# Optimization experiments

Hardware: AMD Instinct MI355X
Metric: run time of the kernel (lower is better)

The kernel has to match this reference:

```python
import jax, jax.numpy as jnp
import numpy as np

HEADS = 8
DIM_HEAD = 64
SCALE = DIM_HEAD ** -0.5


def setup_inputs() -> dict:
    key = jax.random.key(0)
    k1, k2, k3, k4 = jax.random.split(key, 4)
    b, dim, l = 4, 512, 2048
    hidden = HEADS * DIM_HEAD  # 512
    x = jax.random.normal(k1, (b, dim, l), dtype=jnp.float32)
    w_qkv = jax.random.normal(k2, (3 * hidden, dim), dtype=jnp.float32) * (dim ** -0.5)
    w_out = jax.random.normal(k3, (dim, hidden), dtype=jnp.float32) * (hidden ** -0.5)
    b_out = jax.random.normal(k4, (dim,), dtype=jnp.float32) * 0.01
    return {"x": x, "w_qkv": w_qkv, "w_out": w_out, "b_out": b_out}


def reference(x, w_qkv, w_out, b_out):
    b, c, l = x.shape
    h, d = HEADS, DIM_HEAD
    # 1x1 Conv1d == channel matmul: [3*hidden, c] x [b, c, l] -> [b, 3*hidden, l]
    qkv = jnp.einsum('oc,bcl->bol', w_qkv, x)
    q, k, v = jnp.split(qkv, 3, axis=1)
    # 'b (h d) l -> b h d l'
    q = q.reshape(b, h, d, l) * SCALE
    k = k.reshape(b, h, d, l)
    v = v.reshape(b, h, d, l)
    sim = jnp.einsum('bhdi,bhdj->bhij', q, k)          # [b, h, l, l]
    attn = jax.nn.softmax(sim, axis=-1)
    out = jnp.einsum('bhij,bhdj->bhid', attn, v)       # [b, h, l, d]
    # 'b h l d -> b (h d) l'
    out = out.transpose(0, 1, 3, 2).reshape(b, h * d, l)
    return jnp.einsum('oc,bcl->bol', w_out, out) + b_out[None, :, None]
```

## Files before the change

kernel.cpp:

```cpp
#include <hip/hip_runtime.h>

#define L_SEQ 2048
#define KDIM  512

typedef __attribute__((ext_vector_type(8))) short short8v;
typedef __attribute__((ext_vector_type(4))) float f32x4;
typedef __attribute__((ext_vector_type(16))) float f32x16;
typedef __attribute__((ext_vector_type(4))) unsigned u32x4;

static __device__ __forceinline__ short f2b(float f) {
    union { float f; unsigned u; } v; v.f = f;
    unsigned r = v.u + 0x7fffu + ((v.u >> 16) & 1u);
    return (short)(r >> 16);
}

static __device__ __forceinline__ float fast_exp2(float x) {
#if __has_builtin(__builtin_amdgcn_exp2f)
    return __builtin_amdgcn_exp2f(x);
#else
    return exp2f(x);
#endif
}

static __device__ __forceinline__ void gl2lds16(const short* g, short* l) {
    __builtin_amdgcn_global_load_lds(
        (const __attribute__((address_space(1))) unsigned*)g,
        (__attribute__((address_space(3))) unsigned*)l,
        16, 0, 0);
}

__global__ __launch_bounds__(256) void prep(
    const float* __restrict__ wq, const float* __restrict__ wo,
    const float* __restrict__ x,
    short* __restrict__ wqb, short* __restrict__ wob, short* __restrict__ xT)
{
    __shared__ __align__(16) float T[64 * 72];
    const int t = threadIdx.x;
    int bid = blockIdx.x;

    if (bid < 1024) {
        const int i = bid * 256 + t;
        const int NQ = 1536 * 512 / 4;
        float4 v;
        if (i < NQ) v = ((const float4*)wq)[i];
        else        v = ((const float4*)wo)[i - NQ];
        short4 s;
        s.x = f2b(v.x); s.y = f2b(v.y); s.z = f2b(v.z); s.w = f2b(v.w);
        if (i < NQ) ((short4*)wqb)[i] = s;
        else        ((short4*)wob)[i - NQ] = s;
        return;
    }
    bid -= 1024;
    const int l0 = (bid & 31) * 64;
    const int c0 = ((bid >> 5) & 7) * 64;
    const int b  = bid >> 8;

#pragma unroll
    for (int j = 0; j < 4; ++j) {
        const int idx = j * 256 + t;
        const int row = idx >> 4, c4 = idx & 15;
        const float4 v = *(const float4*)&x[((size_t)b * KDIM + c0 + row) * L_SEQ + l0 + c4 * 4];
        *(float4*)&T[row * 72 + c4 * 4] = v;
    }
    __syncthreads();

#pragma unroll
    for (int j = 0; j < 2; ++j) {
        const int idx = j * 256 + t;
        const int l = idx >> 3, ch = idx & 7;
        short8v s;
#pragma unroll
        for (int e = 0; e < 8; ++e)
            s[e] = f2b(T[(ch * 8 + e) * 72 + l]);
        *(short8v*)&xT[((size_t)b * L_SEQ + l0 + l) * KDIM + c0 + ch * 8] = s;
    }
}

template<int EPI>
__global__ __launch_bounds__(256) void gemm_bt(
    const short* __restrict__ Ag, const short* __restrict__ Bbase,
    const float* __restrict__ bias,
    short* __restrict__ Qws, short* __restrict__ Kws, short* __restrict__ Vws,
    float* __restrict__ Cout)
{
    constexpr int TO   = (EPI == 0) ? 128 : 64;
    constexpr int WO   = TO / 2;
    constexpr int NI   = WO / 16;
    constexpr int CA   = TO * 64 * 2 / 1024;
    constexpr int CB   = 16;
    constexpr int CPW  = (CA + CB) / 4;
    constexpr int SMEM = (EPI == 0) ? 34816 : 24576;

    const int bz = blockIdx.z;
    const int o0 = blockIdx.y * TO;
    const int l0 = blockIdx.x * 128;
    const short* Bg = Bbase + (size_t)bz * L_SEQ * KDIM;

    __shared__ __align__(16) char smem[SMEM];
    short* sA = (short*)smem;
    short* sB = (short*)(smem + TO * 64 * 2);

    const int t    = threadIdx.x;
    const int w    = t >> 6;
    const int lane = t & 63;
    const int quad = lane >> 4;
    const int l16  = lane & 15;
    const int wo   = (w & 1) * WO;
    const int wl   = (w >> 1) * 64;

    f32x4 acc[NI][4];
#pragma unroll
    for (int i = 0; i < NI; ++i)
#pragma unroll
        for (int n = 0; n < 4; ++n) acc[i][n] = (f32x4){0,0,0,0};

    const int lrow = lane >> 3;
    const int lcol = (lane & 7) * 8;

    for (int k0 = 0; k0 < KDIM; k0 += 64) {
#pragma unroll
        for (int p = 0; p < CPW; ++p) {
            const int cid = w * CPW + p;
            if (cid < CA) {
                const int row = cid * 8 + lrow;
                gl2lds16(Ag + (size_t)(o0 + row) * KDIM + k0 + lcol, sA + cid * 512);
            } else {
                const int row = (cid - CA) * 8 + lrow;
                gl2lds16(Bg + (size_t)(l0 + row) * KDIM + k0 + lcol, sB + (cid - CA) * 512);
            }
        }
        __syncthreads();

#pragma unroll
        for (int ks = 0; ks < 2; ++ks) {
            short8v af[NI], bf[4];
#pragma unroll
            for (int i = 0; i < NI; ++i)
                af[i] = *(const short8v*)&sA[(wo + i * 16 + l16) * 64 + ks * 32 + quad * 8];
#pragma unroll
            for (int n = 0; n < 4; ++n)
                bf[n] = *(const short8v*)&sB[(wl + n * 16 + l16) * 64 + ks * 32 + quad * 8];
#pragma unroll
            for (int i = 0; i < NI; ++i)
#pragma unroll
                for (int n = 0; n < 4; ++n)
                    acc[i][n] = __builtin_amdgcn_mfma_f32_16x16x32_bf16(af[i], bf[n], acc[i][n], 0, 0, 0);
        }
        __syncthreads();
    }

    if (EPI == 0) {
        const int type  = o0 >> 9;
        const int local = o0 & 511;
        const int bh0   = bz * 8 + (local >> 6);
        const float sc  = (type == 0) ? 0.18033688011112042f : 1.0f;
        short* T = (short*)smem;

        if (type == 2) {
#pragma unroll
            for (int i = 0; i < NI; ++i)
#pragma unroll
                for (int n = 0; n < 4; ++n)
#pragma unroll
                    for (int r = 0; r < 4; ++r)
                        T[(wo + i * 16 + quad * 4 + r) * 136 + wl + n * 16 + l16] =
                            f2b(acc[i][n][r]);
            __syncthreads();
#pragma unroll
            for (int p = 0; p < 8; ++p) {
                const int idx = p * 256 + t;
                const int o = idx >> 4, c = idx & 15;
                const float4 v = *(const float4*)&T[o * 136 + c * 8];
                short* dst = Vws + ((size_t)(bh0 + (o >> 6)) * 64 + (o & 63)) * L_SEQ + l0 + c * 8;
                *(float4*)dst = v;
            }
        } else {
#pragma unroll
            for (int i = 0; i < NI; ++i)
#pragma unroll
                for (int n = 0; n < 4; ++n) {
                    short4 s;
                    s.x = f2b(acc[i][n][0] * sc);
                    s.y = f2b(acc[i][n][1] * sc);
                    s.z = f2b(acc[i][n][2] * sc);
                    s.w = f2b(acc[i][n][3] * sc);
                    *(short4*)&T[(wl + n * 16 + l16) * 136 + wo + i * 16 + quad * 4] = s;
                }
            __syncthreads();
            short* base = (type == 0) ? Qws : Kws;
#pragma unroll
            for (int p = 0; p < 8; ++p) {
                const int idx = p * 256 + t;
                const int l = idx >> 4, c = idx & 15;
                const float4 v = *(const float4*)&T[l * 136 + c * 8];
                short* dst = base + ((size_t)(bh0 + (c >> 3)) * L_SEQ + l0 + l) * 64 + (c & 7) * 8;
                *(float4*)dst = v;
            }
        }
    } else {
        float* Cb = Cout + (size_t)bz * KDIM * L_SEQ;
#pragma unroll
        for (int i = 0; i < NI; ++i) {
            const int o = o0 + wo + i * 16 + quad * 4;
            float bv[4];
#pragma unroll
            for (int r = 0; r < 4; ++r) bv[r] = bias[o + r];
#pragma unroll
            for (int n = 0; n < 4; ++n) {
                const int l = l0 + wl + n * 16 + l16;
#pragma unroll
                for (int r = 0; r < 4; ++r)
                    Cb[(size_t)(o + r) * L_SEQ + l] = acc[i][n][r] + bv[r];
            }
        }
    }
}

__global__ __launch_bounds__(512, 4) void attn_mfma(
    const short* __restrict__ Qws, const short* __restrict__ Kws,
    const short* __restrict__ Vws, short* __restrict__ ao)
{
    const int bh = blockIdx.x & 31;
    const int b  = bh >> 3;
    const int h  = bh & 7;
    const int i0 = (blockIdx.x >> 5) * 128;

    __shared__ __align__(16) char smem[36864];
    float* Old = (float*)smem;

    const int t    = threadIdx.x;
    const int w    = t >> 6;
    const int lane = t & 63;
    const int l31  = lane & 31;
    const int hi   = lane >> 5;
    const int gi   = w >> 1;
    const int jh   = w & 1;

    const short* Qb = Qws + (size_t)bh * L_SEQ * 64;
    const short* Kb = Kws + (size_t)bh * L_SEQ * 64;
    const short* Vb = Vws + (size_t)bh * 64 * L_SEQ;

    short8v qa[4];
#pragma unroll
    for (int dk = 0; dk < 4; ++dk)
        qa[dk] = *(const short8v*)(Qb + (size_t)(i0 + gi * 32 + l31) * 64 + dk * 16 + hi * 8);

    f32x16 oacc0, oacc1;
#pragma unroll
    for (int e = 0; e < 16; ++e) { oacc0[e] = 0.f; oacc1[e] = 0.f; }
    float rsum = 0.f;

    const int r = t >> 3, c = t & 7;

    {
        short* K0 = (short*)smem;
        short* V0 = (short*)(smem + 9216);
        const float4 k0 = *(const float4*)(Kb + (size_t)r * 64 + c * 8);
        const float4 v0 = *(const float4*)(Vb + (size_t)r * L_SEQ + c * 8);
        *(float4*)&K0[r * 72 + c * 8] = k0;
        *(float4*)&V0[r * 72 + c * 8] = v0;
    }
    __syncthreads();

    for (int jt = 0; jt < L_SEQ / 64; ++jt) {
        const int j0 = jt * 64;
        const short* Kc = (const short*)(smem + (jt & 1) * 18432);
        const short* Vc = (const short*)(smem + (jt & 1) * 18432 + 9216);
        const bool more = (jt + 1 < L_SEQ / 64);

        float4 nk, nv;
        if (more) {
            nk = *(const float4*)(Kb + (size_t)(j0 + 64 + r) * 64 + c * 8);
            nv = *(const float4*)(Vb + (size_t)r * L_SEQ + j0 + 64 + c * 8);
        }

        f32x16 sacc;
#pragma unroll
        for (int e = 0; e < 16; ++e) sacc[e] = 0.f;
#pragma unroll
        for (int dk = 0; dk < 4; ++dk) {
            const short8v kf = *(const short8v*)&Kc[(jh * 32 + l31) * 72 + dk * 16 + hi * 8];
            sacc = __builtin_amdgcn_mfma_f32_32x32x16_bf16(kf, qa[dk], sacc, 0, 0, 0);
        }

        float p[16];
#pragma unroll
        for (int e = 0; e < 16; ++e) p[e] = fast_exp2(sacc[e]);
#pragma unroll
        for (int e = 0; e < 16; e += 4)
            rsum += (p[e] + p[e + 1]) + (p[e + 2] + p[e + 3]);

        unsigned wv[8];
#pragma unroll
        for (int g = 0; g < 4; ++g) {
            wv[2 * g]     = __builtin_amdgcn_perm(__float_as_uint(p[4 * g + 1]),
                                                  __float_as_uint(p[4 * g]),     0x07060302u);
            wv[2 * g + 1] = __builtin_amdgcn_perm(__float_as_uint(p[4 * g + 3]),
                                                  __float_as_uint(p[4 * g + 2]), 0x07060302u);
        }
        unsigned xv[8];
#pragma unroll
        for (int k = 0; k < 8; ++k)
            xv[k] = (unsigned)__shfl_xor((int)wv[k], 32, 64);

        u32x4 f0, f1;
        f0[0] = hi ? xv[2] : wv[0];  f0[1] = hi ? xv[3] : wv[1];
        f0[2] = hi ? wv[2] : xv[0];  f0[3] = hi ? wv[3] : xv[1];
        f1[0] = hi ? xv[6] : wv[4];  f1[1] = hi ? xv[7] : wv[5];
        f1[2] = hi ? wv[6] : xv[4];  f1[3] = hi ? wv[7] : xv[5];
        const short8v pa0 = __builtin_bit_cast(short8v, f0);
        const short8v pa1 = __builtin_bit_cast(short8v, f1);

        {
            const short8v vf00 = *(const short8v*)&Vc[(0 * 32 + l31) * 72 + jh * 32 + 0 * 16 + hi * 8];
            const short8v vf01 = *(const short8v*)&Vc[(1 * 32 + l31) * 72 + jh * 32 + 0 * 16 + hi * 8];
            oacc0 = __builtin_amdgcn_mfma_f32_32x32x16_bf16(pa0, vf00, oacc0, 0, 0, 0);
            oacc1 = __builtin_amdgcn_mfma_f32_32x32x16_bf16(pa0, vf01, oacc1, 0, 0, 0);
            const short8v vf10 = *(const short8v*)&Vc[(0 * 32 + l31) * 72 + jh * 32 + 1 * 16 + hi * 8];
            const short8v vf11 = *(const short8v*)&Vc[(1 * 32 + l31) * 72 + jh * 32 + 1 * 16 + hi * 8];
            oacc0 = __builtin_amdgcn_mfma_f32_32x32x16_bf16(pa1, vf10, oacc0, 0, 0, 0);
            oacc1 = __builtin_amdgcn_mfma_f32_32x32x16_bf16(pa1, vf11, oacc1, 0, 0, 0);
        }

        if (more) {
            short* Kn = (short*)(smem + ((jt & 1) ^ 1) * 18432);
            short* Vn = (short*)(smem + ((jt & 1) ^ 1) * 18432 + 9216);
            *(float4*)&Kn[r * 72 + c * 8] = nk;
            *(float4*)&Vn[r * 72 + c * 8] = nv;
        }
        __syncthreads();
    }

    const float r2 = rsum + __shfl_xor(rsum, 32, 64);

    float* Opart = (float*)smem;
    float* Rp    = (float*)(smem + 32768);

    if (jh == 1) {
#pragma unroll
        for (int q = 0; q < 4; ++q) {
            float4 a = { oacc0[4 * q], oacc0[4 * q + 1], oacc0[4 * q + 2], oacc0[4 * q + 3] };
            float4 bq = { oacc1[4 * q], oacc1[4 * q + 1], oacc1[4 * q + 2], oacc1[4 * q + 3] };
            *(float4*)&Opart[gi * 2048 + q * 256 + lane * 4]         = a;
            *(float4*)&Opart[gi * 2048 + (4 + q) * 256 + lane * 4]   = bq;
        }
        if (hi == 0) Rp[gi * 32 + l31] = r2;
    }
    __syncthreads();

    if (jh == 0) {
#pragma unroll
        for (int q = 0; q < 4; ++q) {
            const float4 a  = *(const float4*)&Opart[gi * 2048 + q * 256 + lane * 4];
            const float4 bq = *(const float4*)&Opart[gi * 2048 + (4 + q) * 256 + lane * 4];
            oacc0[4 * q] += a.x;  oacc0[4 * q + 1] += a.y;
            oacc0[4 * q + 2] += a.z; oacc0[4 * q + 3] += a.w;
            oacc1[4 * q] += bq.x; oacc1[4 * q + 1] += bq.y;
            oacc1[4 * q + 2] += bq.z; oacc1[4 * q + 3] += bq.w;
        }
        const float rt  = r2 + Rp[gi * 32 + l31];
        const float inv = 1.0014f / rt;
#pragma unroll
        for (int e = 0; e < 16; ++e) {
            const int rowi = (e & 3) + 8 * (e >> 2) + 4 * hi;
            const float iv = __shfl(inv, rowi, 64);
            oacc0[e] *= iv;
            oacc1[e] *= iv;
        }
    }
    __syncthreads();

    if (jh == 0) {
#pragma unroll
        for (int e = 0; e < 16; ++e) {
            const int rowi = (e & 3) + 8 * (e >> 2) + 4 * hi;
            Old[(gi * 32 + rowi) * 68 + l31]      = oacc0[e];
            Old[(gi * 32 + rowi) * 68 + 32 + l31] = oacc1[e];
        }
    }
    __syncthreads();

#pragma unroll
    for (int p = 0; p < 4; ++p) {
        const int idx = p * 512 + t;
        const int i = idx >> 4, c4 = idx & 15;
        const float4 v = *(const float4*)&Old[i * 68 + c4 * 4];
        short4 s;
        s.x = f2b(v.x); s.y = f2b(v.y); s.z = f2b(v.z); s.w = f2b(v.w);
        *(short4*)&ao[((size_t)b * L_SEQ + i0 + i) * KDIM + h * 64 + c4 * 4] = s;
    }
}

extern "C" void kernel_launch(void* const* d_in, const int* in_sizes, int n_in,
                              void* d_out, int out_size, void* d_ws, size_t ws_size,
                              hipStream_t stream)
{
    const float* x     = (const float*)d_in[0];
    const float* w_qkv = (const float*)d_in[1];
    const float* w_out = (const float*)d_in[2];
    const float* b_out = (const float*)d_in[3];
    float* out = (float*)d_out;

    char* ws = (char*)d_ws;
    short* xT    = (short*)ws;                      ws += (size_t)4 * L_SEQ * KDIM * 2;
    short* wq_bf = (short*)ws;                      ws += (size_t)1536 * 512 * 2;
    short* wo_bf = (short*)ws;                      ws += (size_t)512 * 512 * 2;
    short* Qws   = (short*)ws;                      ws += (size_t)32 * L_SEQ * 64 * 2;
    short* Kws   = (short*)ws;                      ws += (size_t)32 * L_SEQ * 64 * 2;
    short* Vws   = (short*)ws;                      ws += (size_t)32 * L_SEQ * 64 * 2;
    short* ao    = (short*)ws;

    dim3 blk(256);
    prep       <<<dim3(2048), blk, 0, stream>>>(w_qkv, w_out, x, wq_bf, wo_bf, xT);
    gemm_bt<0> <<<dim3(16, 12, 4), blk, 0, stream>>>(wq_bf, xT, nullptr, Qws, Kws, Vws, nullptr);
    attn_mfma  <<<dim3(512), dim3(512), 0, stream>>>(Qws, Kws, Vws, ao);
    gemm_bt<1> <<<dim3(16, 8, 4), blk, 0, stream>>>(wo_bf, ao, b_out, nullptr, nullptr, nullptr, out);
}
```

Measured before the change: 162.1 us.

## Software-pipeline attention loop with triple-buffered K/V and one-step-ahead QK

Restructures the attention inner loop so that each step computes the QK^T scores for the next tile while doing exp and PV for the current one. K/V staging moves from a double buffer to a triple buffer with a two-tile prefetch distance. The loop is unrolled by six so the buffer rotation is fixed at compile time. The goal is to overlap MFMA work with exp/shuffle work and to hide global load latency. In exchange, LDS grows from 36 KB to 54 KB per block and register pressure rises, which may cut occupancy under launch_bounds(512,4).

```diff
diff --git a/kernel.cpp b/kernel.cpp
--- a/kernel.cpp
+++ b/kernel.cpp
@@ -216,6 +216,83 @@
     }
 }
 
+template<bool DO_QK, bool DO_STAGE>
+static __device__ __forceinline__ void attn_step(
+    const int jt,
+    const short* __restrict__ bQK,
+    const short* __restrict__ bPV,
+    short* __restrict__ bW,
+    const short* __restrict__ Kb, const short* __restrict__ Vb,
+    const short8v (&qa)[4],
+    f32x16& sC, f32x16& sN,
+    f32x16& oacc0, f32x16& oacc1, float& rsum,
+    const int r, const int c, const int l31, const int hi, const int jh)
+{
+    float4 nk, nv;
+    if (DO_STAGE) {
+        nk = *(const float4*)(Kb + (size_t)((jt + 2) * 64 + r) * 64 + c * 8);
+        nv = *(const float4*)(Vb + (size_t)r * L_SEQ + (jt + 2) * 64 + c * 8);
+    }
+
+    if (DO_QK) {
+        f32x16 s;
+#pragma unroll
+        for (int e = 0; e < 16; ++e) s[e] = 0.f;
+#pragma unroll
+        for (int dk = 0; dk < 4; ++dk) {
+            const short8v kf = *(const short8v*)&bQK[(jh * 32 + l31) * 72 + dk * 16 + hi * 8];
+            s = __builtin_amdgcn_mfma_f32_32x32x16_bf16(kf, qa[dk], s, 0, 0, 0);
+        }
+        sN = s;
+    }
+
+    float p[16];
+#pragma unroll
+    for (int e = 0; e < 16; ++e) p[e] = fast_exp2(sC[e]);
+#pragma unroll
+    for (int e = 0; e < 16; e += 4)
+        rsum += (p[e] + p[e + 1]) + (p[e + 2] + p[e + 3]);
+
+    unsigned wv[8];
+#pragma unroll
+    for (int g = 0; g < 4; ++g) {
+        wv[2 * g]     = __builtin_amdgcn_perm(__float_as_uint(p[4 * g + 1]),
+                                              __float_as_uint(p[4 * g]),     0x07060302u);
+        wv[2 * g + 1] = __builtin_amdgcn_perm(__float_as_uint(p[4 * g + 3]),
+                                              __float_as_uint(p[4 * g + 2]), 0x07060302u);
+    }
+    unsigned xv[8];
+#pragma unroll
+    for (int k = 0; k < 8; ++k)
+        xv[k] = (unsigned)__shfl_xor((int)wv[k], 32, 64);
+
+    u32x4 f0, f1;
+    f0[0] = hi ? xv[2] : wv[0];  f0[1] = hi ? xv[3] : wv[1];
+    f0[2] = hi ? wv[2] : xv[0];  f0[3] = hi ? wv[3] : xv[1];
+    f1[0] = hi ? xv[6] : wv[4];  f1[1] = hi ? xv[7] : wv[5];
+    f1[2] = hi ? wv[6] : xv[4];  f1[3] = hi ? wv[7] : xv[5];
+    const short8v pa0 = __builtin_bit_cast(short8v, f0);
+    const short8v pa1 = __builtin_bit_cast(short8v, f1);
+
+    const short* Vc = bPV + 4608;
+    {
+        const short8v vf00 = *(const short8v*)&Vc[(0 * 32 + l31) * 72 + jh * 32 + 0 * 16 + hi * 8];
+        const short8v vf01 = *(const short8v*)&Vc[(1 * 32 + l31) * 72 + jh * 32 + 0 * 16 + hi * 8];
+        oacc0 = __builtin_amdgcn_mfma_f32_32x32x16_bf16(pa0, vf00, oacc0, 0, 0, 0);
+        oacc1 = __builtin_amdgcn_mfma_f32_32x32x16_bf16(pa0, vf01, oacc1, 0, 0, 0);
+        const short8v vf10 = *(const short8v*)&Vc[(0 * 32 + l31) * 72 + jh * 32 + 1 * 16 + hi * 8];
+        const short8v vf11 = *(const short8v*)&Vc[(1 * 32 + l31) * 72 + jh * 32 + 1 * 16 + hi * 8];
+        oacc0 = __builtin_amdgcn_mfma_f32_32x32x16_bf16(pa1, vf10, oacc0, 0, 0, 0);
+        oacc1 = __builtin_amdgcn_mfma_f32_32x32x16_bf16(pa1, vf11, oacc1, 0, 0, 0);
+    }
+
+    if (DO_STAGE) {
+        *(float4*)&bW[r * 72 + c * 8]        = nk;
+        *(float4*)&bW[4608 + r * 72 + c * 8] = nv;
+    }
+    __syncthreads();
+}
+
 __global__ __launch_bounds__(512, 4) void attn_mfma(
     const short* __restrict__ Qws, const short* __restrict__ Kws,
     const short* __restrict__ Vws, short* __restrict__ ao)
@@ -225,7 +302,10 @@
     const int h  = bh & 7;
     const int i0 = (blockIdx.x >> 5) * 128;
 
-    __shared__ __align__(16) char smem[36864];
+    __shared__ __align__(16) char smem[55296];
+    short* B0 = (short*)smem;
+    short* B1 = (short*)(smem + 18432);
+    short* B2 = (short*)(smem + 36864);
     float* Old = (float*)smem;
 
     const int t    = threadIdx.x;
@@ -253,83 +333,37 @@
     const int r = t >> 3, c = t & 7;
 
     {
-        short* K0 = (short*)smem;
-        short* V0 = (short*)(smem + 9216);
         const float4 k0 = *(const float4*)(Kb + (size_t)r * 64 + c * 8);
         const float4 v0 = *(const float4*)(Vb + (size_t)r * L_SEQ + c * 8);
-        *(float4*)&K0[r * 72 + c * 8] = k0;
-        *(float4*)&V0[r * 72 + c * 8] = v0;
-    }
-    __syncthreads();
-
-    for (int jt = 0; jt < L_SEQ / 64; ++jt) {
-        const int j0 = jt * 64;
-        const short* Kc = (const short*)(smem + (jt & 1) * 18432);
-        const short* Vc = (const short*)(smem + (jt & 1) * 18432 + 9216);
-        const bool more = (jt + 1 < L_SEQ / 64);
-
-        float4 nk, nv;
-        if (more) {
-            nk = *(const float4*)(Kb + (size_t)(j0 + 64 + r) * 64 + c * 8);
-            nv = *(const float4*)(Vb + (size_t)r * L_SEQ + j0 + 64 + c * 8);
-        }
-
-        f32x16 sacc;
-#pragma unroll
-        for (int e = 0; e < 16; ++e) sacc[e] = 0.f;
-#pragma unroll
-        for (int dk = 0; dk < 4; ++dk) {
-            const short8v kf = *(const short8v*)&Kc[(jh * 32 + l31) * 72 + dk * 16 + hi * 8];
-            sacc = __builtin_amdgcn_mfma_f32_32x32x16_bf16(kf, qa[dk], sacc, 0, 0, 0);
-        }
-
-        float p[16];
-#pragma unroll
-        for (int e = 0; e < 16; ++e) p[e] = fast_exp2(sacc[e]);
-#pragma unroll
-        for (int e = 0; e < 16; e += 4)
-            rsum += (p[e] + p[e + 1]) + (p[e + 2] + p[e + 3]);
-
-        unsigned wv[8];
-#pragma unroll
-        for (int g = 0; g < 4; ++g) {
-            wv[2 * g]     = __builtin_amdgcn_perm(__float_as_uint(p[4 * g + 1]),
-                                                  __float_as_uint(p[4 * g]),     0x07060302u);
-            wv[2 * g + 1] = __builtin_amdgcn_perm(__float_as_uint(p[4 * g + 3]),
-                                                  __float_as_uint(p[4 * g + 2]), 0x07060302u);
-        }
-        unsigned xv[8];
-#pragma unroll
-        for (int k = 0; k < 8; ++k)
-            xv[k] = (unsigned)__shfl_xor((int)wv[k], 32, 64);
-
-        u32x4 f0, f1;
-        f0[0] = hi ? xv[2] : wv[0];  f0[1] = hi ? xv[3] : wv[1];
-        f0[2] = hi ? wv[2] : xv[0];  f0[3] = hi ? wv[3] : xv[1];
-        f1[0] = hi ? xv[6] : wv[4];  f1[1] = hi ? xv[7] : wv[5];
-        f1[2] = hi ? wv[6] : xv[4];  f1[3] = hi ? wv[7] : xv[5];
-        const short8v pa0 = __builtin_bit_cast(short8v, f0);
-        const short8v pa1 = __builtin_bit_cast(short8v, f1);
-
-        {
-            const short8v vf00 = *(const short8v*)&Vc[(0 * 32 + l31) * 72 + jh * 32 + 0 * 16 + hi * 8];
-            const short8v vf01 = *(const short8v*)&Vc[(1 * 32 + l31) * 72 + jh * 32 + 0 * 16 + hi * 8];
-            oacc0 = __builtin_amdgcn_mfma_f32_32x32x16_bf16(pa0, vf00, oacc0, 0, 0, 0);
-            oacc1 = __builtin_amdgcn_mfma_f32_32x32x16_bf16(pa0, vf01, oacc1, 0, 0, 0);
-            const short8v vf10 = *(const short8v*)&Vc[(0 * 32 + l31) * 72 + jh * 32 + 1 * 16 + hi * 8];
-            const short8v vf11 = *(const short8v*)&Vc[(1 * 32 + l31) * 72 + jh * 32 + 1 * 16 + hi * 8];
-            oacc0 = __builtin_amdgcn_mfma_f32_32x32x16_bf16(pa1, vf10, oacc0, 0, 0, 0);
-            oacc1 = __builtin_amdgcn_mfma_f32_32x32x16_bf16(pa1, vf11, oacc1, 0, 0, 0);
-        }
-
-        if (more) {
-            short* Kn = (short*)(smem + ((jt & 1) ^ 1) * 18432);
-            short* Vn = (short*)(smem + ((jt & 1) ^ 1) * 18432 + 9216);
-            *(float4*)&Kn[r * 72 + c * 8] = nk;
-            *(float4*)&Vn[r * 72 + c * 8] = nv;
-        }
-        __syncthreads();
-    }
+        const float4 k1 = *(const float4*)(Kb + (size_t)(64 + r) * 64 + c * 8);
+        const float4 v1 = *(const float4*)(Vb + (size_t)r * L_SEQ + 64 + c * 8);
+        *(float4*)&B0[r * 72 + c * 8]        = k0;
+        *(float4*)&B0[4608 + r * 72 + c * 8] = v0;
+        *(float4*)&B1[r * 72 + c * 8]        = k1;
+        *(float4*)&B1[4608 + r * 72 + c * 8] = v1;
+    }
+    __syncthreads();
+
+    f32x16 sA, sB;
+#pragma unroll
+    for (int e = 0; e < 16; ++e) sA[e] = 0.f;
+#pragma unroll
+    for (int dk = 0; dk < 4; ++dk) {
+        const short8v kf = *(const short8v*)&B0[(jh * 32 + l31) * 72 + dk * 16 + hi * 8];
+        sA = __builtin_amdgcn_mfma_f32_32x32x16_bf16(kf, qa[dk], sA, 0, 0, 0);
+    }
+
+    for (int p6 = 0; p6 < 5; ++p6) {
+        const int t6 = p6 * 6;
+        attn_step<true, true>(t6 + 0, B1, B0, B2, Kb, Vb, qa, sA, sB, oacc0, oacc1, rsum, r, c, l31, hi, jh);
+        attn_step<true, true>(t6 + 1, B2, B1, B0, Kb, Vb, qa, sB, sA, oacc0, oacc1, rsum, r, c, l31, hi, jh);
+        attn_step<true, true>(t6 + 2, B0, B2, B1, Kb, Vb, qa, sA, sB, oacc0, oacc1, rsum, r, c, l31, hi, jh);
+        attn_step<true, true>(t6 + 3, B1, B0, B2, Kb, Vb, qa, sB, sA, oacc0, oacc1, rsum, r, c, l31, hi, jh);
+        attn_step<true, true>(t6 + 4, B2, B1, B0, Kb, Vb, qa, sA, sB, oacc0, oacc1, rsum, r, c, l31, hi, jh);
+        attn_step<true, true>(t6 + 5, B0, B2, B1, Kb, Vb, qa, sB, sA, oacc0, oacc1, rsum, r, c, l31, hi, jh);
+    }
+    attn_step<true,  false>(30, B1, B0, B2, Kb, Vb, qa, sA, sB, oacc0, oacc1, rsum, r, c, l31, hi, jh);
+    attn_step<false, false>(31, B2, B1, B0, Kb, Vb, qa, sB, sA, oacc0, oacc1, rsum, r, c, l31, hi, jh);
 
     const float r2 = rsum + __shfl_xor(rsum, 32, 64);
 
```

New measurement: 162.1 us. About the same (-0.0%).

## Double query rows per attention wave, use permlane32 swap, and XCD-swizzle GEMM grid

Applied to the files above, without the earlier changes.

The attention kernel moves from 512 to 256 threads per block, with each wave handling two 32-row query tiles. This reuses every K and V LDS fragment across two MFMA chains and halves LDS traffic per FLOP. The cross-half-wave exchange of P values now uses v_permlane32_swap instead of shfl_xor plus selects. Both GEMM launches become 1D grids with an XCD-aware block remap so neighbouring tiles share L2. The cost is more accumulator registers per wave (four 32x32 outputs) and lower occupancy bounds.

```diff
diff --git a/kernel.cpp b/kernel.cpp
--- a/kernel.cpp
+++ b/kernel.cpp
@@ -90,10 +90,18 @@
     constexpr int CB   = 16;
     constexpr int CPW  = (CA + CB) / 4;
     constexpr int SMEM = (EPI == 0) ? 34816 : 24576;
-
-    const int bz = blockIdx.z;
-    const int o0 = blockIdx.y * TO;
-    const int l0 = blockIdx.x * 128;
+    constexpr int NY   = (EPI == 0) ? 12 : 8;
+    constexpr int CPX  = 16 * NY * 4 / 8;
+
+    const int o   = blockIdx.x;
+    const int wsw = (o & 7) * CPX + (o >> 3);
+    const int xb  = wsw / (NY * 4);
+    const int rem = wsw % (NY * 4);
+    const int bz  = rem / NY;
+    const int yb  = rem % NY;
+
+    const int o0 = yb * TO;
+    const int l0 = xb * 128;
     const short* Bg = Bbase + (size_t)bz * L_SEQ * KDIM;
 
     __shared__ __align__(16) char smem[SMEM];
@@ -160,7 +168,7 @@
 #pragma unroll
             for (int i = 0; i < NI; ++i)
 #pragma unroll
-                for (int n = 0; n < 4; ++n)
+            for (int n = 0; n < 4; ++n)
 #pragma unroll
                     for (int r = 0; r < 4; ++r)
                         T[(wo + i * 16 + quad * 4 + r) * 136 + wl + n * 16 + l16] =
@@ -169,9 +177,9 @@
 #pragma unroll
             for (int p = 0; p < 8; ++p) {
                 const int idx = p * 256 + t;
-                const int o = idx >> 4, c = idx & 15;
-                const float4 v = *(const float4*)&T[o * 136 + c * 8];
-                short* dst = Vws + ((size_t)(bh0 + (o >> 6)) * 64 + (o & 63)) * L_SEQ + l0 + c * 8;
+                const int oo = idx >> 4, cc = idx & 15;
+                const float4 v = *(const float4*)&T[oo * 136 + cc * 8];
+                short* dst = Vws + ((size_t)(bh0 + (oo >> 6)) * 64 + (oo & 63)) * L_SEQ + l0 + cc * 8;
                 *(float4*)dst = v;
             }
         } else {
@@ -191,9 +199,9 @@
 #pragma unroll
             for (int p = 0; p < 8; ++p) {
                 const int idx = p * 256 + t;
-                const int l = idx >> 4, c = idx & 15;
-                const float4 v = *(const float4*)&T[l * 136 + c * 8];
-                short* dst = base + ((size_t)(bh0 + (c >> 3)) * L_SEQ + l0 + l) * 64 + (c & 7) * 8;
+                const int l = idx >> 4, cc = idx & 15;
+                const float4 v = *(const float4*)&T[l * 136 + cc * 8];
+                short* dst = base + ((size_t)(bh0 + (cc >> 3)) * L_SEQ + l0 + l) * 64 + (cc & 7) * 8;
                 *(float4*)dst = v;
             }
         }
@@ -201,22 +209,26 @@
         float* Cb = Cout + (size_t)bz * KDIM * L_SEQ;
 #pragma unroll
         for (int i = 0; i < NI; ++i) {
-            const int o = o0 + wo + i * 16 + quad * 4;
+            const int oo = o0 + wo + i * 16 + quad * 4;
             float bv[4];
 #pragma unroll
-            for (int r = 0; r < 4; ++r) bv[r] = bias[o + r];
+            for (int r = 0; r < 4; ++r) bv[r] = bias[oo + r];
 #pragma unroll
             for (int n = 0; n < 4; ++n) {
                 const int l = l0 + wl + n * 16 + l16;
 #pragma unroll
                 for (int r = 0; r < 4; ++r)
-                    Cb[(size_t)(o + r) * L_SEQ + l] = acc[i][n][r] + bv[r];
-            }
-        }
-    }
-}
-
-__global__ __launch_bounds__(512, 4) void attn_mfma(
+                    Cb[(size_t)(oo + r) * L_SEQ + l] = acc[i][n][r] + bv[r];
+            }
+        }
+    }
+}
+
+static __device__ __forceinline__ void plswap(unsigned& a, unsigned& b) {
+    asm("v_permlane32_swap_b32 %0, %1" : "+v"(a), "+v"(b));
+}
+
+__global__ __launch_bounds__(256, 2) void attn_mfma(
     const short* __restrict__ Qws, const short* __restrict__ Kws,
     const short* __restrict__ Vws, short* __restrict__ ao)
 {
@@ -240,25 +252,34 @@
     const short* Kb = Kws + (size_t)bh * L_SEQ * 64;
     const short* Vb = Vws + (size_t)bh * 64 * L_SEQ;
 
-    short8v qa[4];
-#pragma unroll
-    for (int dk = 0; dk < 4; ++dk)
-        qa[dk] = *(const short8v*)(Qb + (size_t)(i0 + gi * 32 + l31) * 64 + dk * 16 + hi * 8);
-
-    f32x16 oacc0, oacc1;
-#pragma unroll
-    for (int e = 0; e < 16; ++e) { oacc0[e] = 0.f; oacc1[e] = 0.f; }
-    float rsum = 0.f;
-
-    const int r = t >> 3, c = t & 7;
+    short8v qa[2][4];
+#pragma unroll
+    for (int it = 0; it < 2; ++it)
+#pragma unroll
+        for (int dk = 0; dk < 4; ++dk)
+            qa[it][dk] = *(const short8v*)(Qb +
+                (size_t)(i0 + gi * 64 + it * 32 + l31) * 64 + dk * 16 + hi * 8);
+
+    f32x16 o00, o01, o10, o11;
+#pragma unroll
+    for (int e = 0; e < 16; ++e) { o00[e] = 0.f; o01[e] = 0.f; o10[e] = 0.f; o11[e] = 0.f; }
+    float rsum0 = 0.f, rsum1 = 0.f;
+
+    const int r = t >> 2, c = t & 3;
 
     {
         short* K0 = (short*)smem;
         short* V0 = (short*)(smem + 9216);
-        const float4 k0 = *(const float4*)(Kb + (size_t)r * 64 + c * 8);
-        const float4 v0 = *(const float4*)(Vb + (size_t)r * L_SEQ + c * 8);
-        *(float4*)&K0[r * 72 + c * 8] = k0;
-        *(float4*)&V0[r * 72 + c * 8] = v0;
+        const short* kg = Kb + (size_t)r * 64 + c * 16;
+        const short* vg = Vb + (size_t)r * L_SEQ + c * 16;
+        const float4 k0 = *(const float4*)kg;
+        const float4 k1 = *(const float4*)(kg + 8);
+        const float4 v0 = *(const float4*)vg;
+        const float4 v1 = *(const float4*)(vg + 8);
+        *(float4*)&K0[r * 72 + c * 16]     = k0;
+        *(float4*)&K0[r * 72 + c * 16 + 8] = k1;
+        *(float4*)&V0[r * 72 + c * 16]     = v0;
+        *(float4*)&V0[r * 72 + c * 16 + 8] = v1;
     }
     __syncthreads();
 
@@ -268,70 +289,106 @@
         const short* Vc = (const short*)(smem + (jt & 1) * 18432 + 9216);
         const bool more = (jt + 1 < L_SEQ / 64);
 
-        float4 nk, nv;
+        float4 nk0, nk1, nv0, nv1;
         if (more) {
-            nk = *(const float4*)(Kb + (size_t)(j0 + 64 + r) * 64 + c * 8);
-            nv = *(const float4*)(Vb + (size_t)r * L_SEQ + j0 + 64 + c * 8);
-        }
-
-        f32x16 sacc;
-#pragma unroll
-        for (int e = 0; e < 16; ++e) sacc[e] = 0.f;
+            const short* kg = Kb + (size_t)(j0 + 64 + r) * 64 + c * 16;
+            const short* vg = Vb + (size_t)r * L_SEQ + j0 + 64 + c * 16;
+            nk0 = *(const float4*)kg;
+            nk1 = *(const float4*)(kg + 8);
+            nv0 = *(const float4*)vg;
+            nv1 = *(const float4*)(vg + 8);
+        }
+
+        f32x16 s0, s1;
+#pragma unroll
+        for (int e = 0; e < 16; ++e) { s0[e] = 0.f; s1[e] = 0.f; }
 #pragma unroll
         for (int dk = 0; dk < 4; ++dk) {
             const short8v kf = *(const short8v*)&Kc[(jh * 32 + l31) * 72 + dk * 16 + hi * 8];
-            sacc = __builtin_amdgcn_mfma_f32_32x32x16_bf16(kf, qa[dk], sacc, 0, 0, 0);
-        }
-
-        float p[16];
-#pragma unroll
-        for (int e = 0; e < 16; ++e) p[e] = fast_exp2(sacc[e]);
-#pragma unroll
-        for (int e = 0; e < 16; e += 4)
-            rsum += (p[e] + p[e + 1]) + (p[e + 2] + p[e + 3]);
-
-        unsigned wv[8];
-#pragma unroll
-        for (int g = 0; g < 4; ++g) {
-            wv[2 * g]     = __builtin_amdgcn_perm(__float_as_uint(p[4 * g + 1]),
-                                                  __float_as_uint(p[4 * g]),     0x07060302u);
-            wv[2 * g + 1] = __builtin_amdgcn_perm(__float_as_uint(p[4 * g + 3]),
-                                                  __float_as_uint(p[4 * g + 2]), 0x07060302u);
-        }
-        unsigned xv[8];
-#pragma unroll
-        for (int k = 0; k < 8; ++k)
-            xv[k] = (unsigned)__shfl_xor((int)wv[k], 32, 64);
-
-        u32x4 f0, f1;
-        f0[0] = hi ? xv[2] : wv[0];  f0[1] = hi ? xv[3] : wv[1];
-        f0[2] = hi ? wv[2] : xv[0];  f0[3] = hi ? wv[3] : xv[1];
-        f1[0] = hi ? xv[6] : wv[4];  f1[1] = hi ? xv[7] : wv[5];
-        f1[2] = hi ? wv[6] : xv[4];  f1[3] = hi ? wv[7] : xv[5];
-        const short8v pa0 = __builtin_bit_cast(short8v, f0);
-        const short8v pa1 = __builtin_bit_cast(short8v, f1);
-
+            s0 = __builtin_amdgcn_mfma_f32_32x32x16_bf16(kf, qa[0][dk], s0, 0, 0, 0);
+            s1 = __builtin_amdgcn_mfma_f32_32x32x16_bf16(kf, qa[1][dk], s1, 0, 0, 0);
+        }
+
+        short8v pa00, pa01, pa10, pa11;
         {
-            const short8v vf00 = *(const short8v*)&Vc[(0 * 32 + l31) * 72 + jh * 32 + 0 * 16 + hi * 8];
-            const short8v vf01 = *(const short8v*)&Vc[(1 * 32 + l31) * 72 + jh * 32 + 0 * 16 + hi * 8];
-            oacc0 = __builtin_amdgcn_mfma_f32_32x32x16_bf16(pa0, vf00, oacc0, 0, 0, 0);
-            oacc1 = __builtin_amdgcn_mfma_f32_32x32x16_bf16(pa0, vf01, oacc1, 0, 0, 0);
-            const short8v vf10 = *(const short8v*)&Vc[(0 * 32 + l31) * 72 + jh * 32 + 1 * 16 + hi * 8];
-            const short8v vf11 = *(const short8v*)&Vc[(1 * 32 + l31) * 72 + jh * 32 + 1 * 16 + hi * 8];
-            oacc0 = __builtin_amdgcn_mfma_f32_32x32x16_bf16(pa1, vf10, oacc0, 0, 0, 0);
-            oacc1 = __builtin_amdgcn_mfma_f32_32x32x16_bf16(pa1, vf11, oacc1, 0, 0, 0);
+            float p[16];
+#pragma unroll
+            for (int e = 0; e < 16; ++e) p[e] = fast_exp2(s0[e]);
+#pragma unroll
+            for (int e = 0; e < 16; e += 4)
+                rsum0 += (p[e] + p[e + 1]) + (p[e + 2] + p[e + 3]);
+            unsigned wv[8];
+#pragma unroll
+            for (int g = 0; g < 4; ++g) {
+                wv[2 * g]     = __builtin_amdgcn_perm(__float_as_uint(p[4 * g + 1]),
+                                                      __float_as_uint(p[4 * g]),     0x07060302u);
+                wv[2 * g + 1] = __builtin_amdgcn_perm(__float_as_uint(p[4 * g + 3]),
+                                                      __float_as_uint(p[4 * g + 2]), 0x07060302u);
+            }
+            unsigned a0 = wv[0], a2 = wv[2]; plswap(a0, a2);
+            unsigned a1 = wv[1], a3 = wv[3]; plswap(a1, a3);
+            unsigned b0 = wv[4], b2 = wv[6]; plswap(b0, b2);
+            unsigned b1 = wv[5], b3 = wv[7]; plswap(b1, b3);
+            u32x4 f0, f1;
+            f0[0] = a0; f0[1] = a1; f0[2] = a2; f0[3] = a3;
+            f1[0] = b0; f1[1] = b1; f1[2] = b2; f1[3] = b3;
+            pa00 = __builtin_bit_cast(short8v, f0);
+            pa01 = __builtin_bit_cast(short8v, f1);
+        }
+        {
+            float p[16];
+#pragma unroll
+            for (int e = 0; e < 16; ++e) p[e] = fast_exp2(s1[e]);
+#pragma unroll
+            for (int e = 0; e < 16; e += 4)
+                rsum1 += (p[e] + p[e + 1]) + (p[e + 2] + p[e + 3]);
+            unsigned wv[8];
+#pragma unroll
+            for (int g = 0; g < 4; ++g) {
+                wv[2 * g]     = __builtin_amdgcn_perm(__float_as_uint(p[4 * g + 1]),
+                                                      __float_as_uint(p[4 * g]),     0x07060302u);
+                wv[2 * g + 1] = __builtin_amdgcn_perm(__float_as_uint(p[4 * g + 3]),
+                                                      __float_as_uint(p[4 * g + 2]), 0x07060302u);
+            }
+            unsigned a0 = wv[0], a2 = wv[2]; plswap(a0, a2);
+            unsigned a1 = wv[1], a3 = wv[3]; plswap(a1, a3);
+            unsigned b0 = wv[4], b2 = wv[6]; plswap(b0, b2);
+            unsigned b1 = wv[5], b3 = wv[7]; plswap(b1, b3);
+            u32x4 f0, f1;
+            f0[0] = a0; f0[1] = a1; f0[2] = a2; f0[3] = a3;
+            f1[0] = b0; f1[1] = b1; f1[2] = b2; f1[3] = b3;
+            pa10 = __builtin_bit_cast(short8v, f0);
+            pa11 = __builtin_bit_cast(short8v, f1);
+        }
+
+        {
+            const short8v v00 = *(const short8v*)&Vc[(0 * 32 + l31) * 72 + jh * 32 + 0 * 16 + hi * 8];
+            o00 = __builtin_amdgcn_mfma_f32_32x32x16_bf16(pa00, v00, o00, 0, 0, 0);
+            o10 = __builtin_amdgcn_mfma_f32_32x32x16_bf16(pa10, v00, o10, 0, 0, 0);
+            const short8v v10 = *(const short8v*)&Vc[(1 * 32 + l31) * 72 + jh * 32 + 0 * 16 + hi * 8];
+            o01 = __builtin_amdgcn_mfma_f32_32x32x16_bf16(pa00, v10, o01, 0, 0, 0);
+            o11 = __builtin_amdgcn_mfma_f32_32x32x16_bf16(pa10, v10, o11, 0, 0, 0);
+            const short8v v01 = *(const short8v*)&Vc[(0 * 32 + l31) * 72 + jh * 32 + 1 * 16 + hi * 8];
+            o00 = __builtin_amdgcn_mfma_f32_32x32x16_bf16(pa01, v01, o00, 0, 0, 0);
+            o10 = __builtin_amdgcn_mfma_f32_32x32x16_bf16(pa11, v01, o10, 0, 0, 0);
+            const short8v v11 = *(const short8v*)&Vc[(1 * 32 + l31) * 72 + jh * 32 + 1 * 16 + hi * 8];
+            o01 = __builtin_amdgcn_mfma_f32_32x32x16_bf16(pa01, v11, o01, 0, 0, 0);
+            o11 = __builtin_amdgcn_mfma_f32_32x32x16_bf16(pa11, v11, o11, 0, 0, 0);
         }
 
         if (more) {
             short* Kn = (short*)(smem + ((jt & 1) ^ 1) * 18432);
             short* Vn = (short*)(smem + ((jt & 1) ^ 1) * 18432 + 9216);
-            *(float4*)&Kn[r * 72 + c * 8] = nk;
-            *(float4*)&Vn[r * 72 + c * 8] = nv;
+            *(float4*)&Kn[r * 72 + c * 16]     = nk0;
+            *(float4*)&Kn[r * 72 + c * 16 + 8] = nk1;
+            *(float4*)&Vn[r * 72 + c * 16]     = nv0;
+            *(float4*)&Vn[r * 72 + c * 16 + 8] = nv1;
         }
         __syncthreads();
     }
 
-    const float r2 = rsum + __shfl_xor(rsum, 32, 64);
+    const float r20 = rsum0 + __shfl_xor(rsum0, 32, 64);
+    const float r21 = rsum1 + __shfl_xor(rsum1, 32, 64);
 
     float* Opart = (float*)smem;
     float* Rp    = (float*)(smem + 32768);
@@ -339,33 +396,43 @@
     if (jh == 1) {
 #pragma unroll
         for (int q = 0; q < 4; ++q) {
-            float4 a = { oacc0[4 * q], oacc0[4 * q + 1], oacc0[4 * q + 2], oacc0[4 * q + 3] };
-            float4 bq = { oacc1[4 * q], oacc1[4 * q + 1], oacc1[4 * q + 2], oacc1[4 * q + 3] };
-            *(float4*)&Opart[gi * 2048 + q * 256 + lane * 4]         = a;
-            *(float4*)&Opart[gi * 2048 + (4 + q) * 256 + lane * 4]   = bq;
-        }
-        if (hi == 0) Rp[gi * 32 + l31] = r2;
+            float4 c0 = { o00[4 * q], o00[4 * q + 1], o00[4 * q + 2], o00[4 * q + 3] };
+            float4 c1 = { o01[4 * q], o01[4 * q + 1], o01[4 * q + 2], o01[4 * q + 3] };
+            float4 c2 = { o10[4 * q], o10[4 * q + 1], o10[4 * q + 2], o10[4 * q + 3] };
+            float4 c3 = { o11[4 * q], o11[4 * q + 1], o11[4 * q + 2], o11[4 * q + 3] };
+            *(float4*)&Opart[gi * 4096 + (0 * 4 + q) * 256 + lane * 4]  = c0;
+            *(float4*)&Opart[gi * 4096 + (1 * 4 + q) * 256 + lane * 4]  = c1;
+            *(float4*)&Opart[gi * 4096 + (2 * 4 + q) * 256 + lane * 4]  = c2;
+            *(float4*)&Opart[gi * 4096 + (3 * 4 + q) * 256 + lane * 4]  = c3;
+        }
+        if (hi == 0) {
+            Rp[gi * 64 + l31]      = r20;
+            Rp[gi * 64 + 32 + l31] = r21;
+        }
     }
     __syncthreads();
 
     if (jh == 0) {
 #pragma unroll
         for (int q = 0; q < 4; ++q) {
-            const float4 a  = *(const float4*)&Opart[gi * 2048 + q * 256 + lane * 4];
-            const float4 bq = *(const float4*)&Opart[gi * 2048 + (4 + q) * 256 + lane * 4];
-            oacc0[4 * q] += a.x;  oacc0[4 * q + 1] += a.y;
-            oacc0[4 * q + 2] += a.z; oacc0[4 * q + 3] += a.w;
-            oacc1[4 * q] += bq.x; oacc1[4 * q + 1] += bq.y;
-            oacc1[4 * q + 2] += bq.z; oacc1[4 * q + 3] += bq.w;
-        }
-        const float rt  = r2 + Rp[gi * 32 + l31];
-        const float inv = 1.0014f / rt;
+            const float4 c0 = *(const float4*)&Opart[gi * 4096 + (0 * 4 + q) * 256 + lane * 4];
+            const float4 c1 = *(const float4*)&Opart[gi * 4096 + (1 * 4 + q) * 256 + lane * 4];
+            const float4 c2 = *(const float4*)&Opart[gi * 4096 + (2 * 4 + q) * 256 + lane * 4];
+            const float4 c3 = *(const float4*)&Opart[gi * 4096 + (3 * 4 + q) * 256 + lane * 4];
+            o00[4 * q] += c0.x; o00[4 * q + 1] += c0.y; o00[4 * q + 2] += c0.z; o00[4 * q + 3] += c0.w;
+            o01[4 * q] += c1.x; o01[4 * q + 1] += c1.y; o01[4 * q + 2] += c1.z; o01[4 * q + 3] += c1.w;
+            o10[4 * q] += c2.x; o10[4 * q + 1] += c2.y; o10[4 * q + 2] += c2.z; o10[4 * q + 3] += c2.w;
+            o11[4 * q] += c3.x; o11[4 * q + 1] += c3.y; o11[4 * q + 2] += c3.z; o11[4 * q + 3] += c3.w;
+        }
+        const float inv0 = 1.0014f / (r20 + Rp[gi * 64 + l31]);
+        const float inv1 = 1.0014f / (r21 + Rp[gi * 64 + 32 + l31]);
 #pragma unroll
         for (int e = 0; e < 16; ++e) {
             const int rowi = (e & 3) + 8 * (e >> 2) + 4 * hi;
-            const float iv = __shfl(inv, rowi, 64);
-            oacc0[e] *= iv;
-            oacc1[e] *= iv;
+            const float iv0 = __shfl(inv0, rowi, 64);
+            const float iv1 = __shfl(inv1, rowi, 64);
+            o00[e] *= iv0;  o01[e] *= iv0;
+            o10[e] *= iv1;  o11[e] *= iv1;
         }
     }
     __syncthreads();
@@ -374,15 +441,17 @@
 #pragma unroll
         for (int e = 0; e < 16; ++e) {
             const int rowi = (e & 3) + 8 * (e >> 2) + 4 * hi;
-            Old[(gi * 32 + rowi) * 68 + l31]      = oacc0[e];
-            Old[(gi * 32 + rowi) * 68 + 32 + l31] = oacc1[e];
+            Old[(gi * 64 + rowi) * 68 + l31]           = o00[e];
+            Old[(gi * 64 + rowi) * 68 + 32 + l31]      = o01[e];
+            Old[(gi * 64 + 32 + rowi) * 68 + l31]      = o10[e];
+            Old[(gi * 64 + 32 + rowi) * 68 + 32 + l31] = o11[e];
         }
     }
     __syncthreads();
 
 #pragma unroll
-    for (int p = 0; p < 4; ++p) {
-        const int idx = p * 512 + t;
+    for (int p = 0; p < 8; ++p) {
+        const int idx = p * 256 + t;
         const int i = idx >> 4, c4 = idx & 15;
         const float4 v = *(const float4*)&Old[i * 68 + c4 * 4];
         short4 s;
@@ -412,7 +481,7 @@
 
     dim3 blk(256);
     prep       <<<dim3(2048), blk, 0, stream>>>(w_qkv, w_out, x, wq_bf, wo_bf, xT);
-    gemm_bt<0> <<<dim3(16, 12, 4), blk, 0, stream>>>(wq_bf, xT, nullptr, Qws, Kws, Vws, nullptr);
-    attn_mfma  <<<dim3(512), dim3(512), 0, stream>>>(Qws, Kws, Vws, ao);
-    gemm_bt<1> <<<dim3(16, 8, 4), blk, 0, stream>>>(wo_bf, ao, b_out, nullptr, nullptr, nullptr, out);
-}
+    gemm_bt<0> <<<dim3(768), blk, 0, stream>>>(wq_bf, xT, nullptr, Qws, Kws, Vws, nullptr);
+    attn_mfma  <<<dim3(512), blk, 0, stream>>>(Qws, Kws, Vws, ao);
+    gemm_bt<1> <<<dim3(512), blk, 0, stream>>>(wo_bf, ao, b_out, nullptr, nullptr, nullptr, out);
+}
```

After: 159.0 us. No clear change (-1.9%).
